# Optimization experiments

Measured on AMD Instinct MI355X. Metric: run time of the kernel, lower is better.

## Reference

```python
import jax, jax.numpy as jnp
import numpy as np

B, C, H, E, K, QT = 256, 1024, 64, 64, 2, 20000

def _mlp(x, W1, b1, W2, b2):
    # GKT MLP (eval mode: dropout off; batch-norm omitted, see notes)
    return jax.nn.relu(jax.nn.relu(x @ W1 + b1) @ W2 + b2)

def setup_inputs() -> dict:
    key = jax.random.key(0)
    ks = jax.random.split(key, 30)
    s = 0.05  # weight scale to keep pre-clamp activations in a sane range
    xt = jax.random.uniform(ks[0], (B,), dtype=jnp.float32)
    qt = jax.random.randint(ks[1], (B,), 0, QT)
    ht = jax.random.normal(ks[2], (B, C, H), dtype=jnp.float32)
    # binary question->concept incidence, ~4 KCs per question, col 0 forced on
    oh = (jax.random.uniform(ks[3], (QT, C)) < 4.0 / C).astype(jnp.float32)
    oh = oh.at[:, 0].set(1.0)
    qt_kc_one_hot = jnp.concatenate([oh, jnp.zeros((1, C), jnp.float32)], axis=0)  # zero padding row
    kc_embeddings = jax.random.normal(ks[4], (C, E), dtype=jnp.float32) * 0.1
    graphs = jax.random.uniform(ks[5], (K, C, C), dtype=jnp.float32)  # graph_model output
    neigh_weight = jnp.float32(0.8)
    MI = H + E
    Ws1 = jax.random.normal(ks[6], (MI, H), jnp.float32) * s; bs1 = jnp.zeros((H,), jnp.float32)
    Ws2 = jax.random.normal(ks[7], (H, H), jnp.float32) * s;  bs2 = jnp.zeros((H,), jnp.float32)
    Wn1 = jax.random.normal(ks[8], (K, 2 * MI, H), jnp.float32) * s; bn1 = jnp.zeros((K, H), jnp.float32)
    Wn2 = jax.random.normal(ks[9], (K, H, H), jnp.float32) * s;      bn2 = jnp.zeros((K, H), jnp.float32)
    ea_w = jax.random.uniform(ks[10], (C,), dtype=jnp.float32)
    We = jax.random.normal(ks[11], (H, H), jnp.float32) * s; be = jnp.zeros((H,), jnp.float32)
    Wa = jax.random.normal(ks[12], (H, H), jnp.float32) * s; ba = jnp.zeros((H,), jnp.float32)
    W_ih = jax.random.normal(ks[13], (H, 3 * H), jnp.float32) * s; b_ih = jnp.zeros((3 * H,), jnp.float32)
    W_hh = jax.random.normal(ks[14], (H, 3 * H), jnp.float32) * s; b_hh = jnp.zeros((3 * H,), jnp.float32)
    Wp = jax.random.normal(ks[15], (H, 1), jnp.float32) * s; bp = jnp.zeros((1,), jnp.float32)
    return dict(xt=xt, qt=qt, ht=ht, qt_kc_one_hot=qt_kc_one_hot, kc_embeddings=kc_embeddings,
                graphs=graphs, neigh_weight=neigh_weight, Ws1=Ws1, bs1=bs1, Ws2=Ws2, bs2=bs2,
                Wn1=Wn1, bn1=bn1, Wn2=Wn2, bn2=bn2, ea_w=ea_w, We=We, be=be, Wa=Wa, ba=ba,
                W_ih=W_ih, b_ih=b_ih, W_hh=W_hh, b_hh=b_hh, Wp=Wp, bp=bp)

def reference(xt, qt, ht, qt_kc_one_hot, kc_embeddings, graphs, neigh_weight,
              Ws1, bs1, Ws2, bs2, Wn1, bn1, Wn2, bn2, ea_w, We, be, Wa, ba,
              W_ih, b_ih, W_hh, b_hh, Wp, bp):
    # ---- _aggregate: the fusion loops never write back, so tmp_ht = cat(ht, kc_emb)
    mask = qt_kc_one_hot[qt]                                   # [B, C] gather of binary incidence
    kc = jnp.broadcast_to(kc_embeddings[None], (mask.shape[0], C, E))
    tmp_ht = jnp.concatenate([ht, kc], axis=-1)                # [B, C, H+E]
    # ---- _agg_neighbors
    self_ht = tmp_ht * mask[..., None]
    self_feat = jnp.clip(_mlp(self_ht, Ws1, bs1, Ws2, bs2), -10.0, 10.0)
    neigh_ht = jnp.clip(jnp.concatenate([self_ht, tmp_ht], axis=-1), -5.0, 5.0)  # [B,C,2(H+E)]
    # bug-faithful adj: mean of graphs[k] rows over sample 0's active concepts
    a0 = mask[0]                                               # [C]
    denom = jnp.maximum(a0.sum(), 1.0)
    adj = jnp.clip(jnp.einsum('c,kcd->kd', a0, graphs) / denom, -5.0, 5.0)       # [K, C]
    nb = jax.vmap(lambda W1, b1, W2, b2: _mlp(neigh_ht, W1, b1, W2, b2))(Wn1, bn1, Wn2, bn2)
    nb = jnp.clip(nb, -5.0, 5.0)                               # [K, B, C, H]
    w = jnp.clip(neigh_weight, 0.1, 0.9)
    nf = jnp.clip(adj[0][None, :, None] * nb[0], -5.0, 5.0)
    for k in range(1, K):
        nf = jnp.clip(w * nf + (1.0 - w) * adj[k][None, :, None] * nb[k], -5.0, 5.0)
    m_next = jnp.clip(jnp.where(mask[..., None] > 0.5, self_feat, nf), -50.0, 50.0)
    # ---- erase-add gate
    g = ea_w[None, :, None]
    res = m_next - g * jax.nn.sigmoid(m_next @ We + be) * m_next + g * jnp.tanh(m_next @ Wa + ba)
    # ---- GRUCell over flattened (B*C) rows
    gi = res @ W_ih + b_ih
    gh = ht @ W_hh + b_hh
    ir, iz, in_ = jnp.split(gi, 3, axis=-1)
    hr, hz, hn = jnp.split(gh, 3, axis=-1)
    r = jax.nn.sigmoid(ir + hr)
    z = jax.nn.sigmoid(iz + hz)
    n = jnp.tanh(in_ + r * hn)
    h_next = (1.0 - z) * n + z * ht                            # [B, C, H]
    y = jax.nn.sigmoid(h_next @ Wp + bp)[..., 0]               # [B, C]
    return y
```

## Files before the change

### kernel.cpp

```cpp
#include <hip/hip_runtime.h>

#define DEVINL __device__ __forceinline__

typedef __bf16 bf16x8 __attribute__((ext_vector_type(8)));
typedef float  f32x4  __attribute__((ext_vector_type(4)));

static constexpr size_t kAdjOff  = 0;
static constexpr size_t kBiasOff = 8192;
static constexpr size_t kFragOff = 8192 + 786432;

static constexpr int FB_Wn1h0 = 0,  FB_Wn1h1 = 8,  FB_Wn2_0 = 16, FB_Wn2_1 = 24;
static constexpr int FB_Ws1h  = 32, FB_Ws2   = 40, FB_We    = 48, FB_Wa    = 56;
static constexpr int FB_Wih   = 64, FB_Whh   = 88;

DEVINL unsigned short bf16r(float f) {
  unsigned u = __builtin_bit_cast(unsigned, f);
  unsigned r = ((u >> 16) & 1u) + 0x7FFFu;
  return (unsigned short)((u + r) >> 16);
}
DEVINL float sigmoidf_(float x) { return __builtin_amdgcn_rcpf(1.f + __expf(-x)); }
DEVINL float tanhf_(float x)    { return 1.f - 2.f * __builtin_amdgcn_rcpf(1.f + __expf(2.f * x)); }

DEVINL void lds_fence() {
  __builtin_amdgcn_sched_barrier(0);
  __builtin_amdgcn_s_waitcnt(0xC07F);
  __builtin_amdgcn_sched_barrier(0);
}

DEVINL f32x4 mfma16(bf16x8 a, bf16x8 b, f32x4 c) {
  return __builtin_amdgcn_mfma_f32_16x16x32_bf16(a, b, c, 0, 0, 0);
}

DEVINL unsigned clip2_(unsigned x) {
  float lo = __builtin_bit_cast(float, x << 16);
  float hi = __builtin_bit_cast(float, x & 0xFFFF0000u);
  lo = fminf(fmaxf(lo, -5.f), 5.f);
  hi = fminf(fmaxf(hi, -5.f), 5.f);
  return (__builtin_bit_cast(unsigned, lo) >> 16) | (__builtin_bit_cast(unsigned, hi) & 0xFFFF0000u);
}
DEVINL bf16x8 clip5(bf16x8 a) {
  uint4 u = __builtin_bit_cast(uint4, a);
  u.x = clip2_(u.x); u.y = clip2_(u.y); u.z = clip2_(u.z); u.w = clip2_(u.w);
  return __builtin_bit_cast(bf16x8, u);
}

__global__ void prep_adj_kernel(const int* __restrict__ qt, const float* __restrict__ onehot,
                                const float* __restrict__ graphs, float* __restrict__ adjw) {
  __shared__ float a0v[1024];
  __shared__ int   aidx[1024];
  __shared__ int   s_nnz;
  __shared__ float s_den;
  const int tid = threadIdx.x;
  const int k = blockIdx.x >> 2, chunk = blockIdx.x & 3;
  if (tid == 0) { s_nnz = 0; s_den = 0.f; }
  __syncthreads();
  const int q0 = qt[0];
  float lsum = 0.f;
#pragma unroll
  for (int i = 0; i < 4; i++) {
    int c = tid * 4 + i;
    float v = onehot[(size_t)q0 * 1024 + c];
    lsum += v;
    if (v != 0.f) { int p = atomicAdd(&s_nnz, 1); aidx[p] = c; a0v[p] = v; }
  }
#pragma unroll
  for (int off = 32; off >= 1; off >>= 1) lsum += __shfl_xor(lsum, off, 64);
  if ((tid & 63) == 0) atomicAdd(&s_den, lsum);
  __syncthreads();
  const float denom = fmaxf(s_den, 1.f);
  const int nnz = s_nnz;
  const int d = chunk * 256 + tid;
  const float* G = graphs + (size_t)k * 1048576 + d;
  float sum = 0.f;
  for (int j = 0; j < nnz; j++) sum += a0v[j] * G[(size_t)aidx[j] * 1024];
  adjw[k * 1024 + d] = fminf(fmaxf(sum / denom, -5.f), 5.f);
}

__global__ void prep_bias_kernel(const float* __restrict__ kc, const float* __restrict__ Wn1,
                                 const float* __restrict__ bn1, const float* __restrict__ Ws1,
                                 const float* __restrict__ bs1, float* __restrict__ biasTab) {
  int gid = blockIdx.x * 256 + threadIdx.x;
  int j = gid & 63;
  int c = (gid >> 6) & 1023;
  int tab = gid >> 16;
  const float* kcr = kc + (size_t)c * 64;
  float s;
  if (tab < 2) {
    s = bn1[tab * 64 + j];
    const float* W = Wn1 + ((size_t)tab * 256 + 192) * 64 + j;
#pragma unroll 4
    for (int e = 0; e < 64; e++) s += fminf(fmaxf(kcr[e], -5.f), 5.f) * W[(size_t)e * 64];
  } else {
    s = bs1[j];
    const float* W = Ws1 + (size_t)64 * 64 + j;
#pragma unroll 4
    for (int e = 0; e < 64; e++) s += kcr[e] * W[(size_t)e * 64];
  }
  int c16 = c >> 4, rr = c & 3, qq = (c & 15) >> 2, nt = j >> 4;
  int lane = qq * 16 + (j & 15);
  biasTab[(size_t)((((c16 * 3 + tab) * 4 + nt) * 64 + lane)) * 4 + rr] = s;
}

__global__ void prep_wfrag_kernel(const float* __restrict__ Wn1, const float* __restrict__ Wn2,
                                  const float* __restrict__ Ws1, const float* __restrict__ Ws2,
                                  const float* __restrict__ We,  const float* __restrict__ Wa,
                                  const float* __restrict__ Wih, const float* __restrict__ Whh,
                                  uint4* __restrict__ wfrag) {
  const int bid = blockIdx.x, lane = threadIdx.x;
  int mat, ks, nt;
  if (bid < 64) { mat = bid >> 3; ks = (bid >> 2) & 1; nt = bid & 3; }
  else { int f2 = bid - 64; mat = 8 + f2 / 24; int f = f2 % 24; ks = f / 12; nt = f % 12; }
  const float* base = Wn1; int stride = 64;
  switch (mat) {
    case 0: base = Wn1 + (size_t)128 * 64; break;
    case 1: base = Wn1 + (size_t)(256 + 128) * 64; break;
    case 2: base = Wn2; break;
    case 3: base = Wn2 + (size_t)64 * 64; break;
    case 4: base = Ws1; break;
    case 5: base = Ws2; break;
    case 6: base = We; break;
    case 7: base = Wa; break;
    case 8: base = Wih; stride = 192; break;
    case 9: base = Whh; stride = 192; break;
  }
  const int qq = lane >> 4, col = nt * 16 + (lane & 15);
  union { unsigned short u[8]; uint4 v; } tmp;
#pragma unroll
  for (int jj = 0; jj < 8; jj++) {
    int k = ks * 32 + qq * 8 + jj;
    tmp.u[jj] = bf16r(base[(size_t)k * stride + col]);
  }
  wfrag[(size_t)bid * 64 + lane] = tmp.v;
}

__global__ __launch_bounds__(256, 2) void gkt_main_kernel(
    const int* __restrict__ qt, const float* __restrict__ onehot, const float* __restrict__ ht,
    const float* __restrict__ nw, const float* __restrict__ bn2, const float* __restrict__ be,
    const float* __restrict__ ba, const float* __restrict__ bih, const float* __restrict__ bhh,
    const float* __restrict__ Wp, const float* __restrict__ bp, const float* __restrict__ eaw,
    const float* __restrict__ bs2, const float* __restrict__ adjw, const float* __restrict__ biasTab,
    const bf16x8* __restrict__ wfrag, float* __restrict__ out) {
  __shared__ __align__(16) unsigned short hbuf[4][32][72];
  __shared__ __align__(16) float tokp[4][128];
  __shared__ __align__(16) uint4 gfrag[48 * 64];

  const int tid = threadIdx.x;
  const int wv = tid >> 6, lane = tid & 63;
  const int q = lane >> 4, cl = lane & 15;
  const int t0 = (blockIdx.x * 4 + wv) * 32;
  const int b = t0 >> 10, c0 = t0 & 1023, c16 = c0 >> 4;

  unsigned short* hb = &hbuf[wv][0][0];
  float* tp = &tokp[wv][0];

  {
    const uint4* wf4 = (const uint4*)wfrag;
#pragma unroll
    for (int i = 0; i < 12; i++) {
      int f = wv * 12 + i;
      gfrag[f * 64 + lane] = wf4[(FB_Wih + f) * 64 + lane];
    }
  }

  if (lane < 32) {
    const int c = c0 + lane;
    tp[lane]      = onehot[(size_t)qt[b] * 1024 + c];
    tp[32 + lane] = adjw[c];
    tp[64 + lane] = adjw[1024 + c];
    tp[96 + lane] = eaw[c];
  }
  {
    const float4* ht4 = (const float4*)ht;
#pragma unroll
    for (int i = 0; i < 8; i++) {
      float4 v = ht4[(size_t)t0 * 16 + i * 64 + lane];
      int e = i * 64 + lane;
      int tok = e >> 4, coll = (e & 15) * 4;
      ushort4 h;
      h.x = bf16r(v.x); h.y = bf16r(v.y); h.z = bf16r(v.z); h.w = bf16r(v.w);
      *(ushort4*)&hbuf[wv][tok][coll] = h;
    }
  }
  __syncthreads();

  const float wmix = fminf(fmaxf(nw[0], 0.1f), 0.9f);
  float wp4[4];
#pragma unroll
  for (int nt = 0; nt < 4; nt++) wp4[nt] = Wp[nt * 16 + cl];
  const float bpv = bp[0];

  auto ldA = [&](int mt, int ks) -> bf16x8 {
    return *(const bf16x8*)(hb + (cl + 16 * mt) * 72 + ks * 32 + q * 8);
  };
  auto ldB = [&](int frag) -> bf16x8 { return wfrag[frag * 64 + lane]; };
  auto ldG = [&](int fr) -> bf16x8 {
    return *(const bf16x8*)&gfrag[fr * 64 + lane];
  };
  auto ldTP4 = [&](int base, int mt) -> f32x4 {
    return *(const f32x4*)(tp + base + 16 * mt + q * 4);
  };
  const f32x4* bt4 = (const f32x4*)biasTab;

  bf16x8 xr[2][2];
#pragma unroll
  for (int mt = 0; mt < 2; mt++)
#pragma unroll
    for (int ks = 0; ks < 2; ks++) xr[mt][ks] = ldA(mt, ks);
  lds_fence();

  f32x4 nf[2][4];
  {
    bf16x8 xc[2][2];
#pragma unroll
    for (int mt = 0; mt < 2; mt++)
#pragma unroll
      for (int ks = 0; ks < 2; ks++) xc[mt][ks] = clip5(xr[mt][ks]);

#pragma unroll
    for (int k2 = 0; k2 < 2; k2++) {
      f32x4 acc[2][4];
#pragma unroll
      for (int mt = 0; mt < 2; mt++)
#pragma unroll
        for (int nt = 0; nt < 4; nt++)
          acc[mt][nt] = bt4[(((c16 + mt) * 3 + k2) * 4 + nt) * 64 + lane];
#pragma unroll
      for (int ks = 0; ks < 2; ks++)
#pragma unroll
        for (int nt = 0; nt < 4; nt++) {
          bf16x8 bb = ldB((k2 ? FB_Wn1h1 : FB_Wn1h0) + ks * 4 + nt);
          acc[0][nt] = mfma16(xc[0][ks], bb, acc[0][nt]);
          acc[1][nt] = mfma16(xc[1][ks], bb, acc[1][nt]);
        }
#pragma unroll
      for (int mt = 0; mt < 2; mt++)
#pragma unroll
        for (int nt = 0; nt < 4; nt++)
#pragma unroll
          for (int r = 0; r < 4; r++)
            hb[(16 * mt + q * 4 + r) * 72 + nt * 16 + cl] = bf16r(fmaxf(acc[mt][nt][r], 0.f));
      lds_fence();
      f32x4 acc2[2][4];
#pragma unroll
      for (int nt = 0; nt < 4; nt++) {
        float bz = bn2[k2 * 64 + nt * 16 + cl];
        f32x4 iv = {bz, bz, bz, bz};
        acc2[0][nt] = iv; acc2[1][nt] = iv;
      }
#pragma unroll
      for (int ks = 0; ks < 2; ks++) {
        bf16x8 a0 = ldA(0, ks), a1 = ldA(1, ks);
#pragma unroll
        for (int nt = 0; nt < 4; nt++) {
          bf16x8 bb = ldB((k2 ? FB_Wn2_1 : FB_Wn2_0) + ks * 4 + nt);
          acc2[0][nt] = mfma16(a0, bb, acc2[0][nt]);
          acc2[1][nt] = mfma16(a1, bb, acc2[1][nt]);
        }
      }
      lds_fence();
#pragma unroll
      for (int mt = 0; mt < 2; mt++) {
        f32x4 adjv = ldTP4((1 + k2) * 32, mt);
#pragma unroll
        for (int nt = 0; nt < 4; nt++)
#pragma unroll
          for (int r = 0; r < 4; r++) {
            float nb = fminf(fmaxf(acc2[mt][nt][r], 0.f), 5.f);
            float v = adjv[r] * nb;
            if (k2 == 0) nf[mt][nt][r] = wmix * fminf(fmaxf(v, -5.f), 5.f);
            else         nf[mt][nt][r] = fminf(fmaxf(nf[mt][nt][r] + (1.f - wmix) * v, -5.f), 5.f);
          }
      }
    }
  }

  bool anySelf = __any((lane < 32) && (tp[lane] > 0.5f));
  if (anySelf) {
    f32x4 acc[2][4];
#pragma unroll
    for (int mt = 0; mt < 2; mt++)
#pragma unroll
      for (int nt = 0; nt < 4; nt++)
        acc[mt][nt] = bt4[(((c16 + mt) * 3 + 2) * 4 + nt) * 64 + lane];
#pragma unroll
    for (int ks = 0; ks < 2; ks++)
#pragma unroll
      for (int nt = 0; nt < 4; nt++) {
        bf16x8 bb = ldB(FB_Ws1h + ks * 4 + nt);
        acc[0][nt] = mfma16(xr[0][ks], bb, acc[0][nt]);
        acc[1][nt] = mfma16(xr[1][ks], bb, acc[1][nt]);
      }
#pragma unroll
    for (int mt = 0; mt < 2; mt++)
#pragma unroll
      for (int nt = 0; nt < 4; nt++)
#pragma unroll
        for (int r = 0; r < 4; r++)
          hb[(16 * mt + q * 4 + r) * 72 + nt * 16 + cl] = bf16r(fmaxf(acc[mt][nt][r], 0.f));
    lds_fence();
    f32x4 acc2[2][4];
#pragma unroll
    for (int nt = 0; nt < 4; nt++) {
      float bz = bs2[nt * 16 + cl];
      f32x4 iv = {bz, bz, bz, bz};
      acc2[0][nt] = iv; acc2[1][nt] = iv;
    }
#pragma unroll
    for (int ks = 0; ks < 2; ks++) {
      bf16x8 a0 = ldA(0, ks), a1 = ldA(1, ks);
#pragma unroll
      for (int nt = 0; nt < 4; nt++) {
        bf16x8 bb = ldB(FB_Ws2 + ks * 4 + nt);
        acc2[0][nt] = mfma16(a0, bb, acc2[0][nt]);
        acc2[1][nt] = mfma16(a1, bb, acc2[1][nt]);
      }
    }
    lds_fence();
#pragma unroll
    for (int mt = 0; mt < 2; mt++) {
      f32x4 mk = ldTP4(0, mt);
#pragma unroll
      for (int nt = 0; nt < 4; nt++)
#pragma unroll
        for (int r = 0; r < 4; r++) {
          float sf = fminf(fmaxf(acc2[mt][nt][r], 0.f), 10.f);
          nf[mt][nt][r] = (mk[r] > 0.5f) ? sf : nf[mt][nt][r];
        }
    }
  }

#pragma unroll
  for (int mt = 0; mt < 2; mt++)
#pragma unroll
    for (int nt = 0; nt < 4; nt++)
#pragma unroll
      for (int r = 0; r < 4; r++)
        hb[(16 * mt + q * 4 + r) * 72 + nt * 16 + cl] = bf16r(nf[mt][nt][r]);
  lds_fence();
  bf16x8 mf[2][2];
#pragma unroll
  for (int mt = 0; mt < 2; mt++)
#pragma unroll
    for (int ks = 0; ks < 2; ks++) mf[mt][ks] = ldA(mt, ks);
  lds_fence();
  {
    f32x4 accE[2][4];
#pragma unroll
    for (int nt = 0; nt < 4; nt++) {
      float bz = be[nt * 16 + cl];
      f32x4 iv = {bz, bz, bz, bz};
      accE[0][nt] = iv; accE[1][nt] = iv;
    }
#pragma unroll
    for (int ks = 0; ks < 2; ks++)
#pragma unroll
      for (int nt = 0; nt < 4; nt++) {
        bf16x8 bb = ldB(FB_We + ks * 4 + nt);
        accE[0][nt] = mfma16(mf[0][ks], bb, accE[0][nt]);
        accE[1][nt] = mfma16(mf[1][ks], bb, accE[1][nt]);
      }
#pragma unroll
    for (int mt = 0; mt < 2; mt++) {
      f32x4 gv = ldTP4(96, mt);
#pragma unroll
      for (int nt = 0; nt < 4; nt++)
#pragma unroll
        for (int r = 0; r < 4; r++) {
          float m = nf[mt][nt][r];
          nf[mt][nt][r] = m - gv[r] * sigmoidf_(accE[mt][nt][r]) * m;
        }
    }
    f32x4 accA[2][4];
#pragma unroll
    for (int nt = 0; nt < 4; nt++) {
      float bz = ba[nt * 16 + cl];
      f32x4 iv = {bz, bz, bz, bz};
      accA[0][nt] = iv; accA[1][nt] = iv;
    }
#pragma unroll
    for (int ks = 0; ks < 2; ks++)
#pragma unroll
      for (int nt = 0; nt < 4; nt++) {
        bf16x8 bb = ldB(FB_Wa + ks * 4 + nt);
        accA[0][nt] = mfma16(mf[0][ks], bb, accA[0][nt]);
        accA[1][nt] = mfma16(mf[1][ks], bb, accA[1][nt]);
      }
#pragma unroll
    for (int mt = 0; mt < 2; mt++) {
      f32x4 gv = ldTP4(96, mt);
#pragma unroll
      for (int nt = 0; nt < 4; nt++)
#pragma unroll
        for (int r = 0; r < 4; r++)
          nf[mt][nt][r] += gv[r] * tanhf_(accA[mt][nt][r]);
    }
  }

#pragma unroll
  for (int mt = 0; mt < 2; mt++)
#pragma unroll
    for (int nt = 0; nt < 4; nt++)
#pragma unroll
      for (int r = 0; r < 4; r++)
        hb[(16 * mt + q * 4 + r) * 72 + nt * 16 + cl] = bf16r(nf[mt][nt][r]);
  lds_fence();
  bf16x8 rf[2][2];
#pragma unroll
  for (int mt = 0; mt < 2; mt++)
#pragma unroll
    for (int ks = 0; ks < 2; ks++) rf[mt][ks] = ldA(mt, ks);

  f32x4 gR[2][4], gZ[2][4], gN[2][4], gH[2][4];
#pragma unroll
  for (int nt = 0; nt < 4; nt++) {
    int col = nt * 16 + cl;
    float brz = bih[col] + bhh[col];
    float bzz = bih[64 + col] + bhh[64 + col];
    float bnn = bih[128 + col];
    float bhn = bhh[128 + col];
    f32x4 v;
    v = {brz, brz, brz, brz}; gR[0][nt] = v; gR[1][nt] = v;
    v = {bzz, bzz, bzz, bzz}; gZ[0][nt] = v; gZ[1][nt] = v;
    v = {bnn, bnn, bnn, bnn}; gN[0][nt] = v; gN[1][nt] = v;
    v = {bhn, bhn, bhn, bhn}; gH[0][nt] = v; gH[1][nt] = v;
  }
#pragma unroll
  for (int ks = 0; ks < 2; ks++)
#pragma unroll
    for (int nt = 0; nt < 4; nt++) {
      bf16x8 bi_r = ldG(ks * 12 + nt);
      bf16x8 bh_r = ldG(24 + ks * 12 + nt);
      bf16x8 bi_z = ldG(ks * 12 + 4 + nt);
      bf16x8 bh_z = ldG(24 + ks * 12 + 4 + nt);
      bf16x8 bi_n = ldG(ks * 12 + 8 + nt);
      bf16x8 bh_n = ldG(24 + ks * 12 + 8 + nt);
#pragma unroll
      for (int mt = 0; mt < 2; mt++) {
        gR[mt][nt] = mfma16(rf[mt][ks], bi_r, gR[mt][nt]);
        gR[mt][nt] = mfma16(xr[mt][ks], bh_r, gR[mt][nt]);
        gZ[mt][nt] = mfma16(rf[mt][ks], bi_z, gZ[mt][nt]);
        gZ[mt][nt] = mfma16(xr[mt][ks], bh_z, gZ[mt][nt]);
        gN[mt][nt] = mfma16(rf[mt][ks], bi_n, gN[mt][nt]);
        gH[mt][nt] = mfma16(xr[mt][ks], bh_n, gH[mt][nt]);
      }
    }

#pragma unroll
  for (int mt = 0; mt < 2; mt++)
#pragma unroll
    for (int r = 0; r < 4; r++) {
      int tok = 16 * mt + q * 4 + r;
      float part = 0.f;
#pragma unroll
      for (int nt = 0; nt < 4; nt++) {
        float rr = sigmoidf_(gR[mt][nt][r]);
        float zz = sigmoidf_(gZ[mt][nt][r]);
        float nval = tanhf_(gN[mt][nt][r] + rr * gH[mt][nt][r]);
        float htv = ht[(size_t)(t0 + tok) * 64 + nt * 16 + cl];
        float hnx = (1.f - zz) * nval + zz * htv;
        part += hnx * wp4[nt];
      }
      part += __shfl_xor(part, 1, 64);
      part += __shfl_xor(part, 2, 64);
      part += __shfl_xor(part, 4, 64);
      part += __shfl_xor(part, 8, 64);
      if (cl == 0) out[t0 + tok] = sigmoidf_(part + bpv);
    }
}

extern "C" void kernel_launch(void* const* d_in, const int* in_sizes, int n_in,
                              void* d_out, int out_size, void* d_ws, size_t ws_size,
                              hipStream_t stream) {
  const int*   qt     = (const int*)d_in[1];
  const float* ht     = (const float*)d_in[2];
  const float* onehot = (const float*)d_in[3];
  const float* kc     = (const float*)d_in[4];
  const float* graphs = (const float*)d_in[5];
  const float* nw     = (const float*)d_in[6];
  const float* Ws1    = (const float*)d_in[7];
  const float* bs1    = (const float*)d_in[8];
  const float* Ws2    = (const float*)d_in[9];
  const float* bs2    = (const float*)d_in[10];
  const float* Wn1    = (const float*)d_in[11];
  const float* bn1    = (const float*)d_in[12];
  const float* Wn2    = (const float*)d_in[13];
  const float* bn2    = (const float*)d_in[14];
  const float* eaw    = (const float*)d_in[15];
  const float* We     = (const float*)d_in[16];
  const float* be     = (const float*)d_in[17];
  const float* Wa     = (const float*)d_in[18];
  const float* ba     = (const float*)d_in[19];
  const float* Wih    = (const float*)d_in[20];
  const float* bih    = (const float*)d_in[21];
  const float* Whh    = (const float*)d_in[22];
  const float* bhh    = (const float*)d_in[23];
  const float* Wp     = (const float*)d_in[24];
  const float* bp     = (const float*)d_in[25];
  float* out = (float*)d_out;

  float* adjw    = (float*)((char*)d_ws + kAdjOff);
  float* biasTab = (float*)((char*)d_ws + kBiasOff);
  uint4* wfragU  = (uint4*)((char*)d_ws + kFragOff);

  prep_adj_kernel<<<8, 256, 0, stream>>>(qt, onehot, graphs, adjw);
  prep_bias_kernel<<<768, 256, 0, stream>>>(kc, Wn1, bn1, Ws1, bs1, biasTab);
  prep_wfrag_kernel<<<112, 64, 0, stream>>>(Wn1, Wn2, Ws1, Ws2, We, Wa, Wih, Whh, wfragU);
  gkt_main_kernel<<<2048, 256, 0, stream>>>(qt, onehot, ht, nw, bn2, be, ba, bih, bhh,
                                            Wp, bp, eaw, bs2, adjw, biasTab,
                                            (const bf16x8*)wfragU, out);
}
```

Baseline: 271.9 us.

## Raise occupancy to three blocks per CU by shrinking LDS and GRU accumulators

Sets launch bounds to three blocks per SM. It cuts the GRU weight fragments staged in LDS from 48 to 32, and the remaining W_hh fragments are read straight from global memory. The GRU gate accumulation is restructured to loop over the two row tiles in turn, which halves the live accumulator registers. The aim is more resident waves to hide latency, at the cost of extra global or L2 fragment loads and possible register spills.

```diff
diff --git a/kernel.cpp b/kernel.cpp
--- a/kernel.cpp
+++ b/kernel.cpp
@@ -133,7 +133,7 @@
   wfrag[(size_t)bid * 64 + lane] = tmp.v;
 }
 
-__global__ __launch_bounds__(256, 2) void gkt_main_kernel(
+__global__ __launch_bounds__(256, 3) void gkt_main_kernel(
     const int* __restrict__ qt, const float* __restrict__ onehot, const float* __restrict__ ht,
     const float* __restrict__ nw, const float* __restrict__ bn2, const float* __restrict__ be,
     const float* __restrict__ ba, const float* __restrict__ bih, const float* __restrict__ bhh,
@@ -142,7 +142,7 @@
     const bf16x8* __restrict__ wfrag, float* __restrict__ out) {
   __shared__ __align__(16) unsigned short hbuf[4][32][72];
   __shared__ __align__(16) float tokp[4][128];
-  __shared__ __align__(16) uint4 gfrag[48 * 64];
+  __shared__ __align__(16) uint4 gfrag[32 * 64];
 
   const int tid = threadIdx.x;
   const int wv = tid >> 6, lane = tid & 63;
@@ -156,9 +156,9 @@
   {
     const uint4* wf4 = (const uint4*)wfrag;
 #pragma unroll
-    for (int i = 0; i < 12; i++) {
-      int f = wv * 12 + i;
-      gfrag[f * 64 + lane] = wf4[(FB_Wih + f) * 64 + lane];
+    for (int i = 0; i < 8; i++) {
+      int f = wv * 8 + i;
+      gfrag[f * 64 + lane] = wf4[(64 + f) * 64 + lane];
     }
   }
 
@@ -194,7 +194,8 @@
   };
   auto ldB = [&](int frag) -> bf16x8 { return wfrag[frag * 64 + lane]; };
   auto ldG = [&](int fr) -> bf16x8 {
-    return *(const bf16x8*)&gfrag[fr * 64 + lane];
+    return (fr < 32) ? *(const bf16x8*)&gfrag[fr * 64 + lane]
+                     : wfrag[(64 + fr) * 64 + lane];
   };
   auto ldTP4 = [&](int base, int mt) -> f32x4 {
     return *(const f32x4*)(tp + base + 16 * mt + q * 4);
@@ -410,52 +411,48 @@
 #pragma unroll
     for (int ks = 0; ks < 2; ks++) rf[mt][ks] = ldA(mt, ks);
 
-  f32x4 gR[2][4], gZ[2][4], gN[2][4], gH[2][4];
-#pragma unroll
-  for (int nt = 0; nt < 4; nt++) {
-    int col = nt * 16 + cl;
-    float brz = bih[col] + bhh[col];
-    float bzz = bih[64 + col] + bhh[64 + col];
-    float bnn = bih[128 + col];
-    float bhn = bhh[128 + col];
-    f32x4 v;
-    v = {brz, brz, brz, brz}; gR[0][nt] = v; gR[1][nt] = v;
-    v = {bzz, bzz, bzz, bzz}; gZ[0][nt] = v; gZ[1][nt] = v;
-    v = {bnn, bnn, bnn, bnn}; gN[0][nt] = v; gN[1][nt] = v;
-    v = {bhn, bhn, bhn, bhn}; gH[0][nt] = v; gH[1][nt] = v;
-  }
-#pragma unroll
-  for (int ks = 0; ks < 2; ks++)
+#pragma unroll
+  for (int mt = 0; mt < 2; mt++) {
+    f32x4 gR[4], gZ[4], gN[4], gH[4];
 #pragma unroll
     for (int nt = 0; nt < 4; nt++) {
-      bf16x8 bi_r = ldG(ks * 12 + nt);
-      bf16x8 bh_r = ldG(24 + ks * 12 + nt);
-      bf16x8 bi_z = ldG(ks * 12 + 4 + nt);
-      bf16x8 bh_z = ldG(24 + ks * 12 + 4 + nt);
-      bf16x8 bi_n = ldG(ks * 12 + 8 + nt);
-      bf16x8 bh_n = ldG(24 + ks * 12 + 8 + nt);
-#pragma unroll
-      for (int mt = 0; mt < 2; mt++) {
-        gR[mt][nt] = mfma16(rf[mt][ks], bi_r, gR[mt][nt]);
-        gR[mt][nt] = mfma16(xr[mt][ks], bh_r, gR[mt][nt]);
-        gZ[mt][nt] = mfma16(rf[mt][ks], bi_z, gZ[mt][nt]);
-        gZ[mt][nt] = mfma16(xr[mt][ks], bh_z, gZ[mt][nt]);
-        gN[mt][nt] = mfma16(rf[mt][ks], bi_n, gN[mt][nt]);
-        gH[mt][nt] = mfma16(xr[mt][ks], bh_n, gH[mt][nt]);
-      }
-    }
-
-#pragma unroll
-  for (int mt = 0; mt < 2; mt++)
+      int col = nt * 16 + cl;
+      float brz = bih[col] + bhh[col];
+      float bzz = bih[64 + col] + bhh[64 + col];
+      float bnn = bih[128 + col];
+      float bhn = bhh[128 + col];
+      gR[nt] = {brz, brz, brz, brz};
+      gZ[nt] = {bzz, bzz, bzz, bzz};
+      gN[nt] = {bnn, bnn, bnn, bnn};
+      gH[nt] = {bhn, bhn, bhn, bhn};
+    }
+#pragma unroll
+    for (int ks = 0; ks < 2; ks++)
+#pragma unroll
+      for (int nt = 0; nt < 4; nt++) {
+        bf16x8 bi_r = ldG(ks * 12 + nt);
+        bf16x8 bh_r = ldG(24 + ks * 12 + nt);
+        bf16x8 bi_z = ldG(ks * 12 + 4 + nt);
+        bf16x8 bh_z = ldG(24 + ks * 12 + 4 + nt);
+        bf16x8 bi_n = ldG(ks * 12 + 8 + nt);
+        bf16x8 bh_n = ldG(24 + ks * 12 + 8 + nt);
+        gR[nt] = mfma16(rf[mt][ks], bi_r, gR[nt]);
+        gR[nt] = mfma16(xr[mt][ks], bh_r, gR[nt]);
+        gZ[nt] = mfma16(rf[mt][ks], bi_z, gZ[nt]);
+        gZ[nt] = mfma16(xr[mt][ks], bh_z, gZ[nt]);
+        gN[nt] = mfma16(rf[mt][ks], bi_n, gN[nt]);
+        gH[nt] = mfma16(xr[mt][ks], bh_n, gH[nt]);
+      }
+
 #pragma unroll
     for (int r = 0; r < 4; r++) {
       int tok = 16 * mt + q * 4 + r;
       float part = 0.f;
 #pragma unroll
       for (int nt = 0; nt < 4; nt++) {
-        float rr = sigmoidf_(gR[mt][nt][r]);
-        float zz = sigmoidf_(gZ[mt][nt][r]);
-        float nval = tanhf_(gN[mt][nt][r] + rr * gH[mt][nt][r]);
+        float rr = sigmoidf_(gR[nt][r]);
+        float zz = sigmoidf_(gZ[nt][r]);
+        float nval = tanhf_(gN[nt][r] + rr * gH[nt][r]);
         float htv = ht[(size_t)(t0 + tok) * 64 + nt * 16 + cl];
         float hnx = (1.f - zz) * nval + zz * htv;
         part += hnx * wp4[nt];
@@ -466,6 +463,7 @@
       part += __shfl_xor(part, 8, 64);
       if (cl == 0) out[t0 + tok] = sigmoidf_(part + bpv);
     }
+  }
 }
 
 extern "C" void kernel_launch(void* const* d_in, const int* in_sizes, int n_in,
```

Measured after the change: 283.3 us. 4.2% more time.
